# Kernel optimization log

Measured on AMD Instinct MI355X. Metric: run time of the kernel, lower is better.

## Reference

```python
import jax, jax.numpy as jnp
import numpy as np

N_R = 256          # number of relations
N_HOP_MAX = 3      # max hops
N_E = 200_000      # number of entities
N_T = 1_000_000    # number of KB triples
B = 32             # batch size
D_Q = 768          # BERT question embedding dim
D_IN = D_Q + (N_HOP_MAX - 1) * N_R  # input width of dense_inf / dense_att


def setup_inputs() -> dict:
    key = jax.random.key(0)
    ks = jax.random.split(key, 7)
    x = (jax.random.uniform(ks[0], (B, N_E)) < 0.001).astype(jnp.float32)
    h_q = jax.random.normal(ks[1], (B, D_Q), jnp.float32)
    W_inf = jax.random.normal(ks[2], (N_R, D_IN), jnp.float32) * 0.02
    W_att = jax.random.normal(ks[3], (1, D_IN), jnp.float32) * 0.02
    subj_idx = jax.random.randint(ks[4], (N_T,), 0, N_E, jnp.int32)
    rel_idx = jax.random.randint(ks[5], (N_T,), 0, N_R, jnp.int32)
    obj_idx = jax.random.randint(ks[6], (N_T,), 0, N_E, jnp.int32)
    return {"x": x, "h_q": h_q, "W_inf": W_inf, "W_att": W_att,
            "subj_idx": subj_idx, "rel_idx": rel_idx, "obj_idx": obj_idx,
            "n_hop": N_HOP_MAX}


def _one_step(x, r, subj_idx, rel_idx, obj_idx):
    # Equivalent to ((x @ M_subj.T) * (r @ M_rel.T)) @ M_obj with 0/1
    # indicator matrices: gather - elementwise multiply - scatter-add.
    x_t = jnp.take(x, subj_idx, axis=1)   # (B, N_T)
    r_t = jnp.take(r, rel_idx, axis=1)    # (B, N_T)
    prod = x_t * r_t                       # (B, N_T)
    # scatter-add over triples into object entities: (N_T, B) -> (N_E, B)
    return jax.ops.segment_sum(prod.T, obj_idx, num_segments=x.shape[1]).T


def reference(x, h_q, W_inf, W_att, subj_idx, rel_idx, obj_idx, n_hop):
    rs, cs, xs = [], [], []
    for i in range(n_hop):
        if i:
            # most-recent relation first, then older ones (rs[::-1])
            concat = jnp.concatenate([h_q] + rs[::-1], axis=1)
        else:
            concat = h_q
        pad = jnp.zeros((h_q.shape[0], (N_HOP_MAX - 1 - i) * N_R), h_q.dtype)
        concat = jnp.concatenate([concat, pad], axis=1)  # (B, D_IN)
        r = concat @ W_inf.T   # (B, N_R)
        c = concat @ W_att.T   # (B, 1)
        x = _one_step(x, r, subj_idx, rel_idx, obj_idx)  # (B, N_E)
        rs.append(r)
        cs.append(c)
        xs.append(x)
    a = jax.nn.softmax(jnp.concatenate(cs, axis=1), axis=-1)  # (B, n_hop)
    y = jnp.einsum('bh,bhe->be', a, jnp.stack(xs, axis=1))     # (B, N_E)
    return y
```

## Files before the change

kernel.cpp:

```cpp
#include <hip/hip_runtime.h>

#define N_R   256
#define N_E   200000
#define N_T   1000000
#define D_Q   768
#define D_IN  1280

template <bool BN>
__device__ __forceinline__ void hop_quad(
        const float* __restrict__ xIn, const unsigned* __restrict__ maskIn,
        const float* __restrict__ rT,
        const int4* __restrict__ subj4, const int4* __restrict__ rel4,
        const int4* __restrict__ obj4,
        float* __restrict__ xOut, unsigned* __restrict__ maskOut,
        int gb, int t) {
    int tid = gb * 256 + t;
    if (tid >= N_T / 4) return;
    int4 s4 = subj4[tid];
    unsigned m0 = maskIn[s4.x], m1 = maskIn[s4.y];
    unsigned m2 = maskIn[s4.z], m3 = maskIn[s4.w];
    if (!(m0 | m1 | m2 | m3)) return;
    int4 r4 = rel4[tid];
    int4 o4 = obj4[tid];
    int      ss[4] = {s4.x, s4.y, s4.z, s4.w};
    unsigned mk[4] = {m0, m1, m2, m3};
    int      rr[4] = {r4.x, r4.y, r4.z, r4.w};
    int      oo[4] = {o4.x, o4.y, o4.z, o4.w};
#pragma unroll
    for (int k = 0; k < 4; ++k) {
        unsigned mm = mk[k];
        if (!mm) continue;
        int s = ss[k], o = oo[k];
        const float* rrow = rT + rr[k] * 32;
        while (mm) {
            int bb = __ffs(mm) - 1;
            mm &= mm - 1;
            float v = BN ? xIn[(size_t)bb * N_E + s] : xIn[(size_t)s * 32 + bb];
            unsafeAtomicAdd(&xOut[(size_t)o * 32 + bb], v * rrow[bb]);
        }
        atomicOr(&maskOut[o], mk[k]);
    }
}

__global__ void kA(const float* __restrict__ x, const float* __restrict__ h_q,
                   const float* __restrict__ W_inf,
                   unsigned* __restrict__ mask0, unsigned* __restrict__ mask1,
                   unsigned* __restrict__ mask2,
                   float4* __restrict__ outv, float* __restrict__ rT0) {
    __shared__ float hs[32 * 257];
    __shared__ float red[256];
    int t = threadIdx.x;
    if (blockIdx.x < 782) {
        int tid = blockIdx.x * 256 + t;
        float4 z = {0.f, 0.f, 0.f, 0.f};
        for (int i = tid; i < 1600000; i += 782 * 256) outv[i] = z;
        if (tid < N_E) {
            unsigned m = 0;
#pragma unroll 8
            for (int b = 0; b < 32; ++b)
                m |= (x[(size_t)b * N_E + tid] != 0.f ? 1u : 0u) << b;
            mask0[tid] = m;
            mask1[tid] = 0u;
            mask2[tid] = 0u;
        }
    } else {
        int rel = blockIdx.x - 782;
        int b = t & 31, kp = t >> 5;
        float acc = 0.f;
        for (int c = 0; c < 3; ++c) {
            __syncthreads();
#pragma unroll
            for (int i = 0; i < 32; ++i)
                hs[i * 257 + t] = h_q[i * D_Q + c * 256 + t];
            __syncthreads();
            const float* w = &W_inf[rel * D_IN + c * 256 + kp * 32];
#pragma unroll
            for (int i = 0; i < 32; ++i)
                acc += w[i] * hs[b * 257 + kp * 32 + i];
        }
        red[t] = acc;
        __syncthreads();
        if (t < 32) {
            float s = 0.f;
            for (int q = 0; q < 8; ++q) s += red[q * 32 + t];
            rT0[rel * 32 + t] = s;
        }
    }
}

__global__ void kB(const float* __restrict__ W_inf, const float* __restrict__ rT0,
                   float* __restrict__ rT1,
                   const float* __restrict__ x, const unsigned* __restrict__ mask0,
                   const int4* __restrict__ subj4, const int4* __restrict__ rel4,
                   const int4* __restrict__ obj4,
                   float* __restrict__ bufA, unsigned* __restrict__ mask1) {
    __shared__ float red[256];
    int t = threadIdx.x;
    if (blockIdx.x < 256) {
        int relb = blockIdx.x;
        int b = t & 31, jp = t >> 5;
        const float* w2 = &W_inf[relb * D_IN + D_Q];
        float acc = 0.f;
#pragma unroll 8
        for (int jj = 0; jj < 32; ++jj) {
            int j = jp * 32 + jj;
            acc += w2[j] * rT0[j * 32 + b];
        }
        red[t] = acc;
        __syncthreads();
        if (t < 32) {
            float s = rT0[relb * 32 + t];
            for (int q = 0; q < 8; ++q) s += red[q * 32 + t];
            rT1[relb * 32 + t] = s;
        }
    } else {
        hop_quad<true>(x, mask0, rT0, subj4, rel4, obj4, bufA, mask1,
                       blockIdx.x - 256, t);
    }
}

__global__ void kC(const float* __restrict__ W_inf, const float* __restrict__ W_att,
                   const float* __restrict__ h_q,
                   const float* __restrict__ rT0, const float* __restrict__ rT1,
                   float* __restrict__ rT2, float* __restrict__ a_w,
                   const float* __restrict__ bufA, const unsigned* __restrict__ mask1,
                   const int4* __restrict__ subj4, const int4* __restrict__ rel4,
                   const int4* __restrict__ obj4,
                   float* __restrict__ bufB, unsigned* __restrict__ mask2) {
    __shared__ float red[256];
    __shared__ float p0[256], p1[256], p2[256], p3[256];
    int t = threadIdx.x;
    if (blockIdx.x < 256) {
        int relb = blockIdx.x;
        int b = t & 31, jp = t >> 5;
        const float* w2 = &W_inf[relb * D_IN + D_Q];
        const float* w3 = w2 + N_R;
        float acc = 0.f;
#pragma unroll 8
        for (int jj = 0; jj < 32; ++jj) {
            int j = jp * 32 + jj;
            acc += w2[j] * rT1[j * 32 + b] + w3[j] * rT0[j * 32 + b];
        }
        red[t] = acc;
        __syncthreads();
        if (t < 32) {
            float s = rT0[relb * 32 + t];
            for (int q = 0; q < 8; ++q) s += red[q * 32 + t];
            rT2[relb * 32 + t] = s;
        }
    } else if (blockIdx.x == 256) {
        int b = t & 31, p = t >> 5;
        float c0 = 0.f;
        for (int k = p * 96; k < p * 96 + 96; ++k) c0 += W_att[k] * h_q[b * D_Q + k];
        float s1 = 0.f, s2 = 0.f, s3 = 0.f;
        for (int j = p * 32; j < p * 32 + 32; ++j) {
            float w2 = W_att[D_Q + j], w3 = W_att[D_Q + N_R + j];
            float r0v = rT0[j * 32 + b], r1v = rT1[j * 32 + b];
            s1 += w2 * r0v; s2 += w2 * r1v; s3 += w3 * r0v;
        }
        p0[t] = c0; p1[t] = s1; p2[t] = s2; p3[t] = s3;
        __syncthreads();
        if (t < 32) {
            float C0 = 0.f, S1 = 0.f, S2 = 0.f, S3 = 0.f;
            for (int q = 0; q < 8; ++q) {
                C0 += p0[q * 32 + t]; S1 += p1[q * 32 + t];
                S2 += p2[q * 32 + t]; S3 += p3[q * 32 + t];
            }
            float c1 = C0 + S1, c2 = C0 + S2 + S3;
            float m  = fmaxf(C0, fmaxf(c1, c2));
            float e0 = __expf(C0 - m), e1 = __expf(c1 - m), e2 = __expf(c2 - m);
            float inv = 1.f / (e0 + e1 + e2);
            a_w[t] = e0 * inv; a_w[32 + t] = e1 * inv; a_w[64 + t] = e2 * inv;
        }
    } else {
        hop_quad<false>(bufA, mask1, rT1, subj4, rel4, obj4, bufB, mask2,
                        blockIdx.x - 257, t);
    }
}

__global__ void kDE(const float* __restrict__ bufA, const float* __restrict__ bufB,
                    const unsigned* __restrict__ mask1,
                    const unsigned* __restrict__ mask2,
                    const float* __restrict__ rT2, const float* __restrict__ a_w,
                    const int4* __restrict__ subj4, const int4* __restrict__ rel4,
                    const int4* __restrict__ obj4, float* __restrict__ out) {
    __shared__ float a0s[32], a1s[32], a2s[32];
    int t = threadIdx.x;
    if (t < 32) { a0s[t] = a_w[t]; a1s[t] = a_w[32 + t]; a2s[t] = a_w[64 + t]; }
    __syncthreads();
    if (blockIdx.x < 977) {
        int tid = blockIdx.x * 256 + t;
        if (tid >= N_T / 4) return;
        int4 s4 = subj4[tid];
        unsigned m0 = mask2[s4.x], m1 = mask2[s4.y];
        unsigned m2 = mask2[s4.z], m3 = mask2[s4.w];
        if (!(m0 | m1 | m2 | m3)) return;
        int4 r4 = rel4[tid];
        int4 o4 = obj4[tid];
        int      ss[4] = {s4.x, s4.y, s4.z, s4.w};
        unsigned mk[4] = {m0, m1, m2, m3};
        int      rr[4] = {r4.x, r4.y, r4.z, r4.w};
        int      oo[4] = {o4.x, o4.y, o4.z, o4.w};
#pragma unroll
        for (int k = 0; k < 4; ++k) {
            unsigned mm = mk[k];
            if (!mm) continue;
            const float* rrow = rT2 + rr[k] * 32;
            const float* xrow = bufB + (size_t)ss[k] * 32;
            int o = oo[k];
            while (mm) {
                int bb = __ffs(mm) - 1;
                mm &= mm - 1;
                unsafeAtomicAdd(&out[(size_t)bb * N_E + o],
                                a2s[bb] * xrow[bb] * rrow[bb]);
            }
        }
    } else {
        int e = (blockIdx.x - 977) * 256 + t;
        if (e >= N_E) return;
        unsigned m1v = mask1[e], m2v = mask2[e];
        unsigned mu = m1v | m2v;
        if (!mu) return;
        const float* r1 = bufA + (size_t)e * 32;
        const float* r2 = bufB + (size_t)e * 32;
        while (mu) {
            int bb = __ffs(mu) - 1;
            mu &= mu - 1;
            float c = 0.f;
            if ((m1v >> bb) & 1) c += a0s[bb] * r1[bb];
            if ((m2v >> bb) & 1) c += a1s[bb] * r2[bb];
            unsafeAtomicAdd(&out[(size_t)bb * N_E + e], c);
        }
    }
}

extern "C" void kernel_launch(void* const* d_in, const int* in_sizes, int n_in,
                              void* d_out, int out_size, void* d_ws, size_t ws_size,
                              hipStream_t stream) {
    const float* x     = (const float*)d_in[0];
    const float* h_q   = (const float*)d_in[1];
    const float* W_inf = (const float*)d_in[2];
    const float* W_att = (const float*)d_in[3];
    const int*   subj  = (const int*)d_in[4];
    const int*   rel   = (const int*)d_in[5];
    const int*   obj   = (const int*)d_in[6];
    float* out = (float*)d_out;

    const size_t NEB = (size_t)N_E * 32;
    float*    bufA  = (float*)d_ws;
    float*    bufB  = bufA + NEB;
    float*    rT0   = bufB + NEB;
    float*    rT1   = rT0 + N_R * 32;
    float*    rT2   = rT1 + N_R * 32;
    float*    a_w   = rT2 + N_R * 32;
    unsigned* mask0 = (unsigned*)(a_w + 96);
    unsigned* mask1 = mask0 + N_E;
    unsigned* mask2 = mask1 + N_E;

    kA<<<782 + 256, 256, 0, stream>>>(x, h_q, W_inf, mask0, mask1, mask2,
                                      (float4*)out, rT0);
    kB<<<256 + 977, 256, 0, stream>>>(W_inf, rT0, rT1, x, mask0,
                                      (const int4*)subj, (const int4*)rel,
                                      (const int4*)obj, bufA, mask1);
    kC<<<257 + 977, 256, 0, stream>>>(W_inf, W_att, h_q, rT0, rT1, rT2, a_w,
                                      bufA, mask1, (const int4*)subj,
                                      (const int4*)rel, (const int4*)obj,
                                      bufB, mask2);
    kDE<<<977 + 782, 256, 0, stream>>>(bufA, bufB, mask1, mask2, rT2, a_w,
                                       (const int4*)subj, (const int4*)rel,
                                       (const int4*)obj, out);
}
```

Baseline: 193.4 us.

## Scatter final hop into entity-major buffer, then combine and transpose via LDS

The final hop now scatters into a new entity-major workspace buffer (bufC) instead of atomically adding into the batch-major output with strided addresses. A new kernel kE then combines the three hop results with the softmax weights and transposes through shared memory, writing the output with coalesced stores. The final-hop gather also loads full x and r rows as float4 vectors, and the mask OR is issued before the atomic adds. This adds an extra kernel launch and one more full-size workspace buffer that must be zeroed and re-read, and kE now writes every output element, including zeros.

```diff
diff --git a/kernel.cpp b/kernel.cpp
--- a/kernel.cpp
+++ b/kernel.cpp
@@ -5,6 +5,7 @@
 #define N_T   1000000
 #define D_Q   768
 #define D_IN  1280
+#define NQ    250000
 
 template <bool BN>
 __device__ __forceinline__ void hop_quad(
@@ -15,7 +16,7 @@
         float* __restrict__ xOut, unsigned* __restrict__ maskOut,
         int gb, int t) {
     int tid = gb * 256 + t;
-    if (tid >= N_T / 4) return;
+    if (tid >= NQ) return;
     int4 s4 = subj4[tid];
     unsigned m0 = maskIn[s4.x], m1 = maskIn[s4.y];
     unsigned m2 = maskIn[s4.z], m3 = maskIn[s4.w];
@@ -32,28 +33,49 @@
         if (!mm) continue;
         int s = ss[k], o = oo[k];
         const float* rrow = rT + rr[k] * 32;
+        atomicOr(&maskOut[o], mm);
         while (mm) {
             int bb = __ffs(mm) - 1;
             mm &= mm - 1;
             float v = BN ? xIn[(size_t)bb * N_E + s] : xIn[(size_t)s * 32 + bb];
             unsafeAtomicAdd(&xOut[(size_t)o * 32 + bb], v * rrow[bb]);
         }
-        atomicOr(&maskOut[o], mk[k]);
-    }
+    }
+}
+
+__device__ __forceinline__ void proc_row(unsigned mm, int s, int r, int o,
+        const float* __restrict__ xIn, const float* __restrict__ rT,
+        float* __restrict__ xOut) {
+    if (!mm) return;
+    const float4* xr = (const float4*)(xIn + (size_t)s * 32);
+    const float4* rr = (const float4*)(rT + (size_t)r * 32);
+    float4 X0 = xr[0], X1 = xr[1], X2 = xr[2], X3 = xr[3];
+    float4 X4 = xr[4], X5 = xr[5], X6 = xr[6], X7 = xr[7];
+    float4 R0 = rr[0], R1 = rr[1], R2 = rr[2], R3 = rr[3];
+    float4 R4 = rr[4], R5 = rr[5], R6 = rr[6], R7 = rr[7];
+    float* dst = xOut + (size_t)o * 32;
+#define AG4(G, X, R) \
+    if (mm & (1u << (4*G+0))) unsafeAtomicAdd(dst + 4*G+0, X.x * R.x); \
+    if (mm & (1u << (4*G+1))) unsafeAtomicAdd(dst + 4*G+1, X.y * R.y); \
+    if (mm & (1u << (4*G+2))) unsafeAtomicAdd(dst + 4*G+2, X.z * R.z); \
+    if (mm & (1u << (4*G+3))) unsafeAtomicAdd(dst + 4*G+3, X.w * R.w);
+    AG4(0, X0, R0) AG4(1, X1, R1) AG4(2, X2, R2) AG4(3, X3, R3)
+    AG4(4, X4, R4) AG4(5, X5, R5) AG4(6, X6, R6) AG4(7, X7, R7)
+#undef AG4
 }
 
 __global__ void kA(const float* __restrict__ x, const float* __restrict__ h_q,
                    const float* __restrict__ W_inf,
                    unsigned* __restrict__ mask0, unsigned* __restrict__ mask1,
                    unsigned* __restrict__ mask2,
-                   float4* __restrict__ outv, float* __restrict__ rT0) {
+                   float4* __restrict__ bufC4, float* __restrict__ rT0) {
     __shared__ float hs[32 * 257];
     __shared__ float red[256];
     int t = threadIdx.x;
     if (blockIdx.x < 782) {
         int tid = blockIdx.x * 256 + t;
         float4 z = {0.f, 0.f, 0.f, 0.f};
-        for (int i = tid; i < 1600000; i += 782 * 256) outv[i] = z;
+        for (int i = tid; i < 1600000; i += 782 * 256) bufC4[i] = z;
         if (tid < N_E) {
             unsigned m = 0;
 #pragma unroll 8
@@ -178,59 +200,61 @@
     }
 }
 
-__global__ void kDE(const float* __restrict__ bufA, const float* __restrict__ bufB,
-                    const unsigned* __restrict__ mask1,
-                    const unsigned* __restrict__ mask2,
-                    const float* __restrict__ rT2, const float* __restrict__ a_w,
-                    const int4* __restrict__ subj4, const int4* __restrict__ rel4,
-                    const int4* __restrict__ obj4, float* __restrict__ out) {
-    __shared__ float a0s[32], a1s[32], a2s[32];
-    int t = threadIdx.x;
-    if (t < 32) { a0s[t] = a_w[t]; a1s[t] = a_w[32 + t]; a2s[t] = a_w[64 + t]; }
+__global__ void kD(const float* __restrict__ bufB, const unsigned* __restrict__ mask2,
+                   const float* __restrict__ rT2,
+                   const int4* __restrict__ subj4, const int4* __restrict__ rel4,
+                   const int4* __restrict__ obj4, float* __restrict__ bufC) {
+    int tid = blockIdx.x * 256 + threadIdx.x;
+    if (tid >= NQ) return;
+    int4 s4 = subj4[tid];
+    int4 r4 = rel4[tid];
+    int4 o4 = obj4[tid];
+    unsigned m0 = mask2[s4.x], m1 = mask2[s4.y];
+    unsigned m2 = mask2[s4.z], m3 = mask2[s4.w];
+    if (!(m0 | m1 | m2 | m3)) return;
+    proc_row(m0, s4.x, r4.x, o4.x, bufB, rT2, bufC);
+    proc_row(m1, s4.y, r4.y, o4.y, bufB, rT2, bufC);
+    proc_row(m2, s4.z, r4.z, o4.z, bufB, rT2, bufC);
+    proc_row(m3, s4.w, r4.w, o4.w, bufB, rT2, bufC);
+}
+
+__global__ void kE(const float* __restrict__ bufA, const float* __restrict__ bufB,
+                   const float* __restrict__ bufC,
+                   const unsigned* __restrict__ mask1,
+                   const unsigned* __restrict__ mask2,
+                   const float* __restrict__ a_w, float* __restrict__ out) {
+    __shared__ float tile[256 * 33];
+    __shared__ unsigned m1s[256], m2s[256];
+    __shared__ float aw[96];
+    int t = threadIdx.x;
+    int e0 = blockIdx.x * 256;
+    if (t < 96) aw[t] = a_w[t];
+    {
+        int e = e0 + t;
+        m1s[t] = (e < N_E) ? mask1[e] : 0u;
+        m2s[t] = (e < N_E) ? mask2[e] : 0u;
+    }
     __syncthreads();
-    if (blockIdx.x < 977) {
-        int tid = blockIdx.x * 256 + t;
-        if (tid >= N_T / 4) return;
-        int4 s4 = subj4[tid];
-        unsigned m0 = mask2[s4.x], m1 = mask2[s4.y];
-        unsigned m2 = mask2[s4.z], m3 = mask2[s4.w];
-        if (!(m0 | m1 | m2 | m3)) return;
-        int4 r4 = rel4[tid];
-        int4 o4 = obj4[tid];
-        int      ss[4] = {s4.x, s4.y, s4.z, s4.w};
-        unsigned mk[4] = {m0, m1, m2, m3};
-        int      rr[4] = {r4.x, r4.y, r4.z, r4.w};
-        int      oo[4] = {o4.x, o4.y, o4.z, o4.w};
-#pragma unroll
-        for (int k = 0; k < 4; ++k) {
-            unsigned mm = mk[k];
-            if (!mm) continue;
-            const float* rrow = rT2 + rr[k] * 32;
-            const float* xrow = bufB + (size_t)ss[k] * 32;
-            int o = oo[k];
-            while (mm) {
-                int bb = __ffs(mm) - 1;
-                mm &= mm - 1;
-                unsafeAtomicAdd(&out[(size_t)bb * N_E + o],
-                                a2s[bb] * xrow[bb] * rrow[bb]);
-            }
-        }
-    } else {
-        int e = (blockIdx.x - 977) * 256 + t;
-        if (e >= N_E) return;
-        unsigned m1v = mask1[e], m2v = mask2[e];
-        unsigned mu = m1v | m2v;
-        if (!mu) return;
-        const float* r1 = bufA + (size_t)e * 32;
-        const float* r2 = bufB + (size_t)e * 32;
-        while (mu) {
-            int bb = __ffs(mu) - 1;
-            mu &= mu - 1;
-            float c = 0.f;
-            if ((m1v >> bb) & 1) c += a0s[bb] * r1[bb];
-            if ((m2v >> bb) & 1) c += a1s[bb] * r2[bb];
-            unsafeAtomicAdd(&out[(size_t)bb * N_E + e], c);
-        }
+    size_t base = (size_t)e0 * 32;
+#pragma unroll
+    for (int i = 0; i < 32; ++i) {
+        int idx = i * 256 + t;
+        int el = idx >> 5, b = idx & 31;
+        float v = 0.f;
+        if (e0 + el < N_E) {
+            v = aw[64 + b] * bufC[base + idx];
+            unsigned mm1 = m1s[el], mm2 = m2s[el];
+            if ((mm1 >> b) & 1) v += aw[b]      * bufA[base + idx];
+            if ((mm2 >> b) & 1) v += aw[32 + b] * bufB[base + idx];
+        }
+        tile[el * 33 + b] = v;
+    }
+    __syncthreads();
+    int e = e0 + t;
+    if (e < N_E) {
+#pragma unroll
+        for (int i = 0; i < 32; ++i)
+            out[(size_t)i * N_E + e] = tile[t * 33 + i];
     }
 }
 
@@ -249,7 +273,8 @@
     const size_t NEB = (size_t)N_E * 32;
     float*    bufA  = (float*)d_ws;
     float*    bufB  = bufA + NEB;
-    float*    rT0   = bufB + NEB;
+    float*    bufC  = bufB + NEB;
+    float*    rT0   = bufC + NEB;
     float*    rT1   = rT0 + N_R * 32;
     float*    rT2   = rT1 + N_R * 32;
     float*    a_w   = rT2 + N_R * 32;
@@ -258,7 +283,7 @@
     unsigned* mask2 = mask1 + N_E;
 
     kA<<<782 + 256, 256, 0, stream>>>(x, h_q, W_inf, mask0, mask1, mask2,
-                                      (float4*)out, rT0);
+                                      (float4*)bufC, rT0);
     kB<<<256 + 977, 256, 0, stream>>>(W_inf, rT0, rT1, x, mask0,
                                       (const int4*)subj, (const int4*)rel,
                                       (const int4*)obj, bufA, mask1);
@@ -266,7 +291,7 @@
                                       bufA, mask1, (const int4*)subj,
                                       (const int4*)rel, (const int4*)obj,
                                       bufB, mask2);
-    kDE<<<977 + 782, 256, 0, stream>>>(bufA, bufB, mask1, mask2, rT2, a_w,
-                                       (const int4*)subj, (const int4*)rel,
-                                       (const int4*)obj, out);
-}
+    kD<<<977, 256, 0, stream>>>(bufB, mask2, rT2, (const int4*)subj,
+                                (const int4*)rel, (const int4*)obj, bufC);
+    kE<<<782, 256, 0, stream>>>(bufA, bufB, bufC, mask1, mask2, a_w, out);
+}
```

Result: slower. 208.6 us (+7.9%).
